# Performance work log

Measured on AMD Instinct MI355X. Metric: run time of the kernel, lower is better.

Reference implementation:

```python
import jax, jax.numpy as jnp
import numpy as np

H = 16        # num_attention_heads
KVH = 4       # num_key_value_heads
D = 128       # head_dim
K = 5         # query multiplier k
HID = 2048    # hidden_size = H * D
THETA = 10000.0


def rotate_half(x):
    h = x.shape[-1] // 2
    return jnp.concatenate([-x[..., h:], x[..., :h]], axis=-1)


def setup_inputs() -> dict:
    key = jax.random.key(0)
    ks = jax.random.split(key, 6)
    B, S = 1, 1024
    q_len = S - 1
    hidden_states = jax.random.normal(ks[0], (B, S, HID), jnp.float32)
    prev_hidden_states = jax.random.normal(ks[1], (B, S - 1, HID), jnp.float32)
    causal = jnp.tril(jnp.ones((q_len, q_len), bool))
    attention_mask = jnp.where(causal, 0.0, -1e9).astype(jnp.float32)[None, None]  # (1,1,q,kv)
    position_ids = jnp.arange(q_len, dtype=jnp.int64)[None]  # (1, kv_len)
    Wq = jax.random.normal(ks[2], (HID, H * D * K), jnp.float32) * 0.02
    Wkv = jax.random.normal(ks[3], (2 * HID, 2 * KVH * D), jnp.float32) * 0.02
    Wo = jax.random.normal(ks[4], (HID, HID), jnp.float32) * 0.02
    return {
        'hidden_states': hidden_states,
        'prev_hidden_states': prev_hidden_states,
        'attention_mask': attention_mask,
        'position_ids': position_ids,
        'Wq': Wq,
        'Wkv': Wkv,
        'Wo': Wo,
    }


def reference(hidden_states, prev_hidden_states, attention_mask, position_ids, Wq, Wkv, Wo):
    B = hidden_states.shape[0]  # must be 1 for this module's broadcasting
    # feature-dim concat of previous layer states with shifted current states
    prev = jnp.concatenate([prev_hidden_states, hidden_states[:, :-1]], axis=-1)  # (B, S-1, 2*HID)
    hs = hidden_states[:, 1:]  # training-mode slice -> (B, q_len, HID)
    q_len = hs.shape[1]
    kv_len = prev.shape[1]

    q = hs @ Wq                       # (B, q_len, H*D*K)
    kv = prev @ Wkv                   # (B, kv_len, 2*KVH*D)
    k_st, v_st = jnp.split(kv, 2, axis=-1)

    # faithful raw reshape: (B, q_len, H*D*K) -> (B*K, q_len, H, D) -> (B*K, H, q_len, D)
    q = q.reshape(B * K, -1, H, D).transpose(0, 2, 1, 3)
    k_st = k_st.reshape(B, kv_len, KVH, D).transpose(0, 2, 1, 3)   # (B, KVH, kv, D)
    v_st = v_st.reshape(B, kv_len, KVH, D).transpose(0, 2, 1, 3)

    # RoPE (LlamaRotaryEmbedding)
    inv_freq = 1.0 / (THETA ** (jnp.arange(0, D, 2, dtype=jnp.float32) / D))  # (D/2,)
    freqs = position_ids.astype(jnp.float32)[..., None] * inv_freq            # (B, kv, D/2)
    emb = jnp.concatenate([freqs, freqs], axis=-1)                            # (B, kv, D)
    cos = jnp.cos(emb)[:, None]  # (B, 1, kv, D)
    sin = jnp.sin(emb)[:, None]
    q = q * cos[..., -q_len:, :] + rotate_half(q) * sin[..., -q_len:, :]
    k_st = k_st * cos[..., :kv_len, :] + rotate_half(k_st) * sin[..., :kv_len, :]

    # repeat_kv: (B, KVH, kv, D) -> (B, H, kv, D)
    n_rep = H // KVH
    k_rep = jnp.repeat(k_st, n_rep, axis=1)
    v_rep = jnp.repeat(v_st, n_rep, axis=1)

    # (B*K, H, q, D) @ (B, H, D, kv) -> broadcast over k variants (B==1)
    attn = jnp.matmul(q, jnp.swapaxes(k_rep, -1, -2)) / jnp.sqrt(jnp.float32(D))
    attn = attn + attention_mask
    attn = jax.nn.softmax(attn.astype(jnp.float32), axis=-1).astype(q.dtype)
    out = jnp.matmul(attn, v_rep)                 # (B*K, H, q, D)
    out = out.transpose(0, 2, 1, 3).reshape(B * K, q_len, HID)
    return out @ Wo                                # (B*K, q_len, HID)
```

## Files before the change

kernel.cpp:

```cpp
#include <hip/hip_runtime.h>
#include <cstddef>
#include <cstdint>

#define SQ    1023
#define HIDC  2048
#define NQC   10240
#define NKVC  1024

typedef unsigned short ushort_t;
typedef __bf16 bf16x8 __attribute__((ext_vector_type(8)));
typedef float  f32x4  __attribute__((ext_vector_type(4)));

__device__ __forceinline__ ushort_t f2bf(float x) {
  union { float f; uint32_t u; } v; v.f = x;
  uint32_t r = v.u + 0x7fffu + ((v.u >> 16) & 1u);
  return (ushort_t)(r >> 16);
}

__device__ __forceinline__ ushort_t f2bf_fast(float x) {
  __bf16 b = (__bf16)x;
  return __builtin_bit_cast(ushort_t, b);
}

__device__ __forceinline__ float fexp2(float x) {
  float r;
  asm("v_exp_f32 %0, %1\n\ts_nop 0" : "=v"(r) : "v"(x));
  return r;
}

__device__ __forceinline__ void fexp2x4(float& a, float& b, float& c, float& d) {
  asm("v_exp_f32 %0, %0\n\t"
      "v_exp_f32 %1, %1\n\t"
      "v_exp_f32 %2, %2\n\t"
      "v_exp_f32 %3, %3\n\t"
      "s_nop 0"
      : "+v"(a), "+v"(b), "+v"(c), "+v"(d));
}

__device__ __forceinline__ void tconv_body(const float* __restrict__ in,
                                           ushort_t* __restrict__ out,
                                           int K, int N, int bx, int by,
                                           int tid, float (&t)[32][33]) {
  int n0 = bx * 32, k0 = by * 32;
  int r = tid >> 5, c = tid & 31;
  #pragma unroll
  for (int p = 0; p < 4; ++p)
    t[p * 8 + r][c] = in[(size_t)(k0 + p * 8 + r) * N + n0 + c];
  __syncthreads();
  #pragma unroll
  for (int p = 0; p < 4; ++p)
    out[(size_t)(n0 + p * 8 + r) * K + k0 + c] = f2bf(t[c][p * 8 + r]);
}

__global__ __launch_bounds__(256)
void k_pre(const float* __restrict__ Wq, const float* __restrict__ Wkv,
           const float* __restrict__ Wo, const float* __restrict__ hidden,
           const float* __restrict__ prevh,
           ushort_t* __restrict__ wqt, ushort_t* __restrict__ wkvt,
           ushort_t* __restrict__ wot, ushort_t* __restrict__ hbf,
           ushort_t* __restrict__ akv,
           float* __restrict__ cosT, float* __restrict__ sinT)
{
  __shared__ float tsh[32][33];
  const int tid = threadIdx.x;
  int b = blockIdx.x;
  if (b < 20480) { tconv_body(Wq, wqt, HIDC, NQC, b % 320, b / 320, tid, tsh); return; }
  b -= 20480;
  if (b < 4096)  { tconv_body(Wkv, wkvt, 4096, NKVC, b % 32, b / 32, tid, tsh); return; }
  b -= 4096;
  if (b < 4096)  { tconv_body(Wo, wot, HIDC, HIDC, b % 64, b / 64, tid, tsh); return; }
  b -= 4096;
  if (b < 2046) {
    int i = (b * 256 + tid) * 4;
    if (i >= SQ * 2048) return;
    int r = i >> 11, c = i & 2047;
    float4 h1 = *reinterpret_cast<const float4*>(hidden + (size_t)(r + 1) * 2048 + c);
    float4 h0 = *reinterpret_cast<const float4*>(hidden + (size_t)r * 2048 + c);
    float4 pv = *reinterpret_cast<const float4*>(prevh + (size_t)r * 2048 + c);
    uint2 a, bb, d;
    a.x  = (uint32_t)f2bf(h1.x) | ((uint32_t)f2bf(h1.y) << 16);
    a.y  = (uint32_t)f2bf(h1.z) | ((uint32_t)f2bf(h1.w) << 16);
    bb.x = (uint32_t)f2bf(pv.x) | ((uint32_t)f2bf(pv.y) << 16);
    bb.y = (uint32_t)f2bf(pv.z) | ((uint32_t)f2bf(pv.w) << 16);
    d.x  = (uint32_t)f2bf(h0.x) | ((uint32_t)f2bf(h0.y) << 16);
    d.y  = (uint32_t)f2bf(h0.z) | ((uint32_t)f2bf(h0.w) << 16);
    *reinterpret_cast<uint2*>(hbf + i) = a;
    *reinterpret_cast<uint2*>(akv + (size_t)r * 4096 + c) = bb;
    *reinterpret_cast<uint2*>(akv + (size_t)r * 4096 + 2048 + c) = d;
    return;
  }
  b -= 2046;
  {
    int idx = b * 256 + tid;
    if (idx >= SQ * 64) return;
    int t = idx >> 6, i = idx & 63;
    float inv = powf(10000.0f, -(float)i * (1.0f / 64.0f));
    float f = (float)t * inv;
    cosT[idx] = cosf(f);
    sinT[idx] = sinf(f);
  }
}

__global__ __launch_bounds__(256)
void k_gemms(const ushort_t* __restrict__ hbf, const ushort_t* __restrict__ wqt,
             ushort_t* __restrict__ qbb, const float* __restrict__ cosT,
             const float* __restrict__ sinT,
             const ushort_t* __restrict__ akv, const ushort_t* __restrict__ wkvt,
             float* __restrict__ kvp)
{
  __shared__ __align__(16) ushort_t As[3][128 * 32];
  __shared__ __align__(16) ushort_t Bs[3][128 * 32];

  const int tid  = threadIdx.x;
  const int lane = tid & 63;
  const int w    = tid >> 6;
  const int wm   = w >> 1, wn = w & 1;
  const int fr   = lane & 15;
  const int kg   = (lane >> 4) * 8;
  const int g4   = lane >> 4;
  const int lrow = lane >> 2;
  const int lk   = (lane & 3) * 8;

  if (blockIdx.x < 640) {
    const int Kd = 2048;
    const int m0 = (blockIdx.x / 80) * 128, n0 = (blockIdx.x % 80) * 128;
    const ushort_t* A  = hbf;
    const ushort_t* Bt = wqt;

    f32x4 acc[4][4];
    #pragma unroll
    for (int i = 0; i < 4; ++i)
      #pragma unroll
      for (int j = 0; j < 4; ++j) acc[i][j] = (f32x4){0.f, 0.f, 0.f, 0.f};

    auto STAGE = [&](int b, int k0) {
      #pragma unroll
      for (int c = 0; c < 2; ++c) {
        int ch  = w + c * 4;
        int row = ch * 16 + lrow;
        const ushort_t* ga = A  + (size_t)(m0 + row) * Kd + k0 + lk;
        const ushort_t* gb = Bt + (size_t)(n0 + row) * Kd + k0 + lk;
        __builtin_amdgcn_global_load_lds(
            (const __attribute__((address_space(1))) void*)ga,
            (__attribute__((address_space(3))) void*)(&As[b][0] + ch * 512), 16, 0, 0);
        __builtin_amdgcn_global_load_lds(
            (const __attribute__((address_space(1))) void*)gb,
            (__attribute__((address_space(3))) void*)(&Bs[b][0] + ch * 512), 16, 0, 0);
      }
    };

    const int nt = Kd / 32;
    STAGE(0, 0);
    STAGE(1, 32);

    int cur = 0;
    for (int t = 0; t < nt; ++t) {
      if (t + 1 < nt) {
        asm volatile("s_waitcnt vmcnt(4)" ::: "memory");
      } else {
        asm volatile("s_waitcnt vmcnt(0)" ::: "memory");
      }
      __builtin_amdgcn_s_barrier();
      if (t + 2 < nt) {
        int sb = cur + 2; if (sb >= 3) sb -= 3;
        STAGE(sb, (t + 2) * 32);
      }

      bf16x8 av[4], bv[4];
      #pragma unroll
      for (int mi = 0; mi < 4; ++mi)
        av[mi] = *reinterpret_cast<const bf16x8*>(&As[cur][0] + (wm * 64 + mi * 16 + fr) * 32 + kg);
      #pragma unroll
      for (int nj = 0; nj < 4; ++nj) {
        int colOff = wn * 32 + (nj & 1) * 16 + (nj >> 1) * 64;
        bv[nj] = *reinterpret_cast<const bf16x8*>(&Bs[cur][0] + (colOff + fr) * 32 + kg);
      }
      #pragma unroll
      for (int mi = 0; mi < 4; ++mi)
        #pragma unroll
        for (int nj = 0; nj < 4; ++nj)
          acc[mi][nj] = __builtin_amdgcn_mfma_f32_16x16x32_bf16(av[mi], bv[nj], acc[mi][nj], 0, 0, 0);

      cur = (cur == 2) ? 0 : cur + 1;
    }

    const float sc = 0.1275174485f;
    const int nChunk = n0 >> 11;
    #pragma unroll
    for (int mi = 0; mi < 4; ++mi) {
      #pragma unroll
      for (int r = 0; r < 4; ++r) {
        int gr = m0 + wm * 64 + mi * 16 + g4 * 4 + r;
        if (gr >= SQ) continue;
        int st  = gr * 5 + nChunk;
        int tau = st % 1023;
        const float* ct  = cosT + tau * 64;
        const float* stb = sinT + tau * 64;
        #pragma unroll
        for (int njp = 0; njp < 2; ++njp) {
          int dd = wn * 32 + njp * 16 + fr;
          float c = ct[dd], s = stb[dd];
          float x0 = acc[mi][njp][r];
          float x1 = acc[mi][njp + 2][r];
          size_t base = (size_t)gr * 10240 + n0 + dd;
          qbb[base]      = f2bf_fast((x0 * c - x1 * s) * sc);
          qbb[base + 64] = f2bf_fast((x1 * c + x0 * s) * sc);
        }
      }
    }
  } else {
    const int u = blockIdx.x - 640;
    const int Kd = 4096, M = SQ, N = NKVC, kLen = 1024;
    const int n0 = (u & 7) * 128, m0 = ((u >> 3) & 15) * 64;
    const int kOff = (u >> 7) * kLen;
    float* C = kvp + (size_t)(u >> 7) * M * N;
    ushort_t* As64 = &As[0][0];
    ushort_t* Bs64 = &Bs[0][0];

    const int arow = tid >> 2, aslot = (tid & 3) * 8;
    const int l15 = lane & 15;

    f32x4 acc[2][4];
    #pragma unroll
    for (int i = 0; i < 2; ++i)
      #pragma unroll
      for (int j = 0; j < 4; ++j) acc[i][j] = (f32x4){0.f, 0.f, 0.f, 0.f};

    for (int k0 = kOff; k0 < kOff + kLen; k0 += 32) {
      {
        const ushort_t* ga = akv + (size_t)(m0 + arow) * Kd + k0 + aslot;
        __builtin_amdgcn_global_load_lds(
            (const __attribute__((address_space(1))) void*)ga,
            (__attribute__((address_space(3))) void*)(As64 + w * 512), 16, 0, 0);
      }
      #pragma unroll
      for (int c = 0; c < 2; ++c) {
        int uu = c * 256 + tid;
        const ushort_t* gb = wkvt + (size_t)(n0 + (uu >> 2)) * Kd + k0 + (uu & 3) * 8;
        __builtin_amdgcn_global_load_lds(
            (const __attribute__((address_space(1))) void*)gb,
            (__attribute__((address_space(3))) void*)(Bs64 + (c * 256 + w * 64) * 8), 16, 0, 0);
      }
      __syncthreads();

      bf16x8 av[2], bv[4];
      #pragma unroll
      for (int mi = 0; mi < 2; ++mi)
        av[mi] = *reinterpret_cast<const bf16x8*>(As64 + (wm * 32 + mi * 16 + fr) * 32 + kg);
      #pragma unroll
      for (int nj = 0; nj < 4; ++nj)
        bv[nj] = *reinterpret_cast<const bf16x8*>(Bs64 + (wn * 64 + nj * 16 + fr) * 32 + kg);
      #pragma unroll
      for (int mi = 0; mi < 2; ++mi)
        #pragma unroll
        for (int nj = 0; nj < 4; ++nj)
          acc[mi][nj] = __builtin_amdgcn_mfma_f32_16x16x32_bf16(av[mi], bv[nj], acc[mi][nj], 0, 0, 0);
      __syncthreads();
    }

    #pragma unroll
    for (int mi = 0; mi < 2; ++mi) {
      #pragma unroll
      for (int nj = 0; nj < 4; ++nj) {
        int rbase = m0 + wm * 32 + mi * 16 + g4 * 4;
        int col   = n0 + wn * 64 + nj * 16 + l15;
        #pragma unroll
        for (int r = 0; r < 4; ++r) {
          int gr = rbase + r;
          if (gr < M) C[(size_t)gr * N + col] = acc[mi][nj][r];
        }
      }
    }
  }
}

__global__ __launch_bounds__(256)
void k_kv(const float* __restrict__ kvp, ushort_t* __restrict__ kb,
          ushort_t* __restrict__ vt, const float* __restrict__ cosT,
          const float* __restrict__ sinT)
{
  __shared__ float tile[32][33];
  const int tid = threadIdx.x;
  int b = blockIdx.x;
  if (b < 1023) {
    int idx = b * 256 + tid;
    if (idx >= SQ * 4 * 64) return;
    int d   = idx & 63;
    int kvh = (idx >> 6) & 3;
    int t   = idx >> 8;
    size_t src = (size_t)t * 1024 + kvh * 128 + d;
    float x0 = 0.f, x1 = 0.f;
    #pragma unroll
    for (int z = 0; z < 4; ++z) {
      x0 += kvp[(size_t)z * (SQ * 1024) + src];
      x1 += kvp[(size_t)z * (SQ * 1024) + src + 64];
    }
    float c = cosT[t * 64 + d], s = sinT[t * 64 + d];
    size_t dst = (size_t)t * 512 + kvh * 128 + d;
    kb[dst]      = f2bf(x0 * c - x1 * s);
    kb[dst + 64] = f2bf(x1 * c + x0 * s);
    return;
  }
  b -= 1023;
  {
    int v0 = (b & 15) * 32;
    int t0 = (b >> 4) * 32;
    int r = tid >> 5, c = tid & 31;
    #pragma unroll
    for (int p = 0; p < 4; ++p) {
      int t = t0 + p * 8 + r;
      float s = 0.f;
      if (t < SQ) {
        size_t src = (size_t)t * 1024 + 512 + v0 + c;
        #pragma unroll
        for (int z = 0; z < 4; ++z) s += kvp[(size_t)z * (SQ * 1024) + src];
      }
      tile[p * 8 + r][c] = s;
    }
    __syncthreads();
    #pragma unroll
    for (int p = 0; p < 4; ++p) {
      int v = v0 + p * 8 + r;
      vt[(size_t)v * 1024 + t0 + c] = f2bf(tile[c][p * 8 + r]);
    }
  }
}

__global__ __launch_bounds__(256)
void k_gemm3buf(const ushort_t* __restrict__ A, const ushort_t* __restrict__ Bt,
                float* __restrict__ C, int M, int N, int Kd)
{
  __shared__ __align__(16) ushort_t As[3][128 * 32];
  __shared__ __align__(16) ushort_t Bs[3][128 * 32];

  const int tid  = threadIdx.x;
  const int lane = tid & 63;
  const int w    = tid >> 6;
  const int wm   = w >> 1, wn = w & 1;
  const int fr   = lane & 15;
  const int kg   = (lane >> 4) * 8;
  const int m0   = blockIdx.y * 128, n0 = blockIdx.x * 128;

  const int lrow = lane >> 2;
  const int lk   = (lane & 3) * 8;

  f32x4 acc[4][4];
  #pragma unroll
  for (int i = 0; i < 4; ++i)
    #pragma unroll
    for (int j = 0; j < 4; ++j) acc[i][j] = (f32x4){0.f, 0.f, 0.f, 0.f};

  auto STAGE = [&](int b, int k0) {
    #pragma unroll
    for (int c = 0; c < 2; ++c) {
      int ch  = w + c * 4;
      int row = ch * 16 + lrow;
      const ushort_t* ga = A  + (size_t)(m0 + row) * Kd + k0 + lk;
      const ushort_t* gb = Bt + (size_t)(n0 + row) * Kd + k0 + lk;
      __builtin_amdgcn_global_load_lds(
          (const __attribute__((address_space(1))) void*)ga,
          (__attribute__((address_space(3))) void*)(&As[b][0] + ch * 512), 16, 0, 0);
      __builtin_amdgcn_global_load_lds(
          (const __attribute__((address_space(1))) void*)gb,
          (__attribute__((address_space(3))) void*)(&Bs[b][0] + ch * 512), 16, 0, 0);
    }
  };

  const int nt = Kd / 32;
  STAGE(0, 0);
  STAGE(1, 32);

  int cur = 0;
  for (int t = 0; t < nt; ++t) {
    if (t + 1 < nt) {
      asm volatile("s_waitcnt vmcnt(4)" ::: "memory");
    } else {
      asm volatile("s_waitcnt vmcnt(0)" ::: "memory");
    }
    __builtin_amdgcn_s_barrier();
    if (t + 2 < nt) {
      int sb = cur + 2; if (sb >= 3) sb -= 3;
      STAGE(sb, (t + 2) * 32);
    }

    bf16x8 av[4], bv[4];
    #pragma unroll
    for (int mi = 0; mi < 4; ++mi)
      av[mi] = *reinterpret_cast<const bf16x8*>(&As[cur][0] + (wm * 64 + mi * 16 + fr) * 32 + kg);
    #pragma unroll
    for (int nj = 0; nj < 4; ++nj)
      bv[nj] = *reinterpret_cast<const bf16x8*>(&Bs[cur][0] + (wn * 64 + nj * 16 + fr) * 32 + kg);
    #pragma unroll
    for (int mi = 0; mi < 4; ++mi)
      #pragma unroll
      for (int nj = 0; nj < 4; ++nj)
        acc[mi][nj] = __builtin_amdgcn_mfma_f32_16x16x32_bf16(av[mi], bv[nj], acc[mi][nj], 0, 0, 0);

    cur = (cur == 2) ? 0 : cur + 1;
  }

  #pragma unroll
  for (int mi = 0; mi < 4; ++mi) {
    #pragma unroll
    for (int nj = 0; nj < 4; ++nj) {
      int rbase = m0 + wm * 64 + mi * 16 + (lane >> 4) * 4;
      int col   = n0 + wn * 64 + nj * 16 + fr;
      #pragma unroll
      for (int r = 0; r < 4; ++r) {
        int gr = rbase + r;
        if (gr < M) C[(size_t)gr * N + col] = acc[mi][nj][r];
      }
    }
  }
}

__global__ __launch_bounds__(256)
void k_attn_mfma(const ushort_t* __restrict__ qb, const ushort_t* __restrict__ kb,
                 const ushort_t* __restrict__ vt, ushort_t* __restrict__ oattb)
{
  __shared__ __align__(16) ushort_t Ks[64 * 128];
  __shared__ __align__(16) ushort_t Vs[128 * 64];
  __shared__ __align__(16) ushort_t Ps[4][16 * 64];

  const int tid  = threadIdx.x;
  const int lane = tid & 63;
  const int w    = tid >> 6;
  const int l15  = lane & 15;
  const int g4   = lane >> 4;
  const int gh   = blockIdx.x;
  const int g = gh >> 4, h = gh & 15, kvh = (gh & 15) >> 2;
  const int qt = 15 - blockIdx.y;
  const int t0 = qt * 64;
  const int tq = t0 + w * 16 + l15;

  bf16x8 av[4];
  {
    const ushort_t* qrow = qb + (((size_t)(g * SQ + tq)) * 16 + h) * 128;
    #pragma unroll
    for (int kk = 0; kk < 4; ++kk)
      av[kk] = *reinterpret_cast<const bf16x8*>(qrow + kk * 32 + g4 * 8);
  }

  f32x4 acc[8];
  #pragma unroll
  for (int dt = 0; dt < 8; ++dt) acc[dt] = (f32x4){0.f, 0.f, 0.f, 0.f};
  float lsum = 0.f;
  float m = -1e30f;

  char* pwb = (char*)&Ps[w][0] + l15 * 128;
  const int pswz = (l15 & 7) << 4;

  for (int jt = 0; jt <= qt; ++jt) {
    int u0 = jt * 64;
    #pragma unroll
    for (int i = 0; i < 4; ++i) {
      int c = (w * 4 + i) * 64 + lane;
      int kv = c >> 4, sl = c & 15;
      const ushort_t* srck = kb + (size_t)(u0 + kv) * 512 + kvh * 128 + ((sl ^ (kv & 7)) << 3);
      __builtin_amdgcn_global_load_lds(
          (const __attribute__((address_space(1))) void*)srck,
          (__attribute__((address_space(3))) void*)(Ks + (w * 4 + i) * 512), 16, 0, 0);
      int d = c >> 3, sv = c & 7;
      const ushort_t* srcv = vt + (size_t)(kvh * 128 + d) * 1024 + u0 + ((sv ^ (d & 7)) << 3);
      __builtin_amdgcn_global_load_lds(
          (const __attribute__((address_space(1))) void*)srcv,
          (__attribute__((address_space(3))) void*)(Vs + (w * 4 + i) * 512), 16, 0, 0);
    }
    __syncthreads();

    f32x4 S[4];
    #pragma unroll
    for (int ct = 0; ct < 4; ++ct) S[ct] = (f32x4){0.f, 0.f, 0.f, 0.f};
    #pragma unroll
    for (int ct = 0; ct < 4; ++ct) {
      int kv = ct * 16 + l15;
      #pragma unroll
      for (int kk = 0; kk < 4; ++kk) {
        bf16x8 kvf = *reinterpret_cast<const bf16x8*>(
            Ks + kv * 128 + ((((kk << 2) | g4) ^ (kv & 7)) << 3));
        S[ct] = __builtin_amdgcn_mfma_f32_16x16x32_bf16(kvf, av[kk], S[ct], 0, 0, 0);
      }
    }
    if (jt == qt) {
      #pragma unroll
      for (int ct = 0; ct < 4; ++ct) {
        int ub = u0 + ct * 16 + g4 * 4;
        #pragma unroll
        for (int r = 0; r < 4; ++r)
          if (ub + r > tq) S[ct][r] = -1e30f;
      }
    }
    float a0 = fmaxf(fmaxf(S[0][0], S[0][1]), fmaxf(S[0][2], S[0][3]));
    float a1 = fmaxf(fmaxf(S[1][0], S[1][1]), fmaxf(S[1][2], S[1][3]));
    float a2 = fmaxf(fmaxf(S[2][0], S[2][1]), fmaxf(S[2][2], S[2][3]));
    float a3 = fmaxf(fmaxf(S[3][0], S[3][1]), fmaxf(S[3][2], S[3][3]));
    float tm = fmaxf(fmaxf(a0, a1), fmaxf(a2, a3));
    tm = fmaxf(tm, __shfl_xor(tm, 16));
    tm = fmaxf(tm, __shfl_xor(tm, 32));

    bool need = tm > m + 8.f;
    if (__any(need)) {
      float mn = fmaxf(m, tm);
      float corr = fexp2(m - mn);
      m = mn;
      lsum *= corr;
      #pragma unroll
      for (int dt = 0; dt < 8; ++dt) acc[dt] *= corr;
    }

    float ps = 0.f;
    #pragma unroll
    for (int ct = 0; ct < 4; ++ct) {
      float e0 = S[ct][0] - m;
      float e1 = S[ct][1] - m;
      float e2 = S[ct][2] - m;
      float e3 = S[ct][3] - m;
      fexp2x4(e0, e1, e2, e3);
      ps += (e0 + e1) + (e2 + e3);
      uint2 pv;
      pv.x = (uint32_t)f2bf_fast(e0) | ((uint32_t)f2bf_fast(e1) << 16);
      pv.y = (uint32_t)f2bf_fast(e2) | ((uint32_t)f2bf_fast(e3) << 16);
      *reinterpret_cast<uint2*>(pwb + ((ct * 32 + g4 * 8) ^ pswz)) = pv;
    }
    ps += __shfl_xor(ps, 16);
    ps += __shfl_xor(ps, 32);
    lsum += ps;

    #pragma unroll
    for (int kk = 0; kk < 2; ++kk) {
      bf16x8 pa = *reinterpret_cast<const bf16x8*>(pwb + ((kk * 64 + g4 * 16) ^ pswz));
      #pragma unroll
      for (int dt = 0; dt < 8; ++dt) {
        int d = dt * 16 + l15;
        bf16x8 vv = *reinterpret_cast<const bf16x8*>(
            Vs + d * 64 + ((((kk << 2) | g4) ^ (d & 7)) << 3));
        acc[dt] = __builtin_amdgcn_mfma_f32_16x16x32_bf16(vv, pa, acc[dt], 0, 0, 0);
      }
    }
    __syncthreads();
  }

  if (tq < SQ) {
    float inv = 1.f / lsum;
    ushort_t* dst = oattb + ((size_t)(g * SQ + tq)) * 2048 + h * 128;
    #pragma unroll
    for (int dt = 0; dt < 8; ++dt) {
      uint2 ov;
      ov.x = (uint32_t)f2bf_fast(acc[dt][0] * inv) | ((uint32_t)f2bf_fast(acc[dt][1] * inv) << 16);
      ov.y = (uint32_t)f2bf_fast(acc[dt][2] * inv) | ((uint32_t)f2bf_fast(acc[dt][3] * inv) << 16);
      *reinterpret_cast<uint2*>(dst + dt * 16 + g4 * 4) = ov;
    }
  }
}

extern "C" void kernel_launch(void* const* d_in, const int* in_sizes, int n_in,
                              void* d_out, int out_size, void* d_ws, size_t ws_size,
                              hipStream_t stream) {
  const float* hidden = (const float*)d_in[0];
  const float* prevh  = (const float*)d_in[1];
  const float* Wq     = (const float*)d_in[4];
  const float* Wkv    = (const float*)d_in[5];
  const float* Wo     = (const float*)d_in[6];
  float* out = (float*)d_out;

  char* ws = (char*)d_ws;
  float*    kvp   = (float*)ws;                        ws += (size_t)4 * SQ * 1024 * 4;
  float*    cosT  = (float*)ws;                        ws += (size_t)65472 * 4;
  float*    sinT  = (float*)ws;                        ws += (size_t)65472 * 4;
  ushort_t* qbb   = (ushort_t*)ws;                     ws += (size_t)5120 * 2048 * 2;
  ushort_t* kb    = (ushort_t*)ws;                     ws += (size_t)1024 * 512 * 2;
  ushort_t* vtb   = (ushort_t*)ws;                     ws += (size_t)512 * 1024 * 2;
  ushort_t* hbf   = (ushort_t*)ws;                     ws += (size_t)1024 * 2048 * 2;
  ushort_t* akv   = (ushort_t*)ws;                     ws += (size_t)1024 * 4096 * 2;
  ushort_t* oattb = (ushort_t*)ws;                     ws += (size_t)5120 * 2048 * 2;
  ushort_t* wqt   = (ushort_t*)ws;                     ws += (size_t)10240 * 2048 * 2;
  ushort_t* wkvt  = (ushort_t*)ws;                     ws += (size_t)1024 * 4096 * 2;
  ushort_t* wot   = (ushort_t*)ws;                     ws += (size_t)2048 * 2048 * 2;

  k_pre<<<dim3(20480 + 4096 + 4096 + 2046 + 256), dim3(256), 0, stream>>>(
      Wq, Wkv, Wo, hidden, prevh, wqt, wkvt, wot, hbf, akv, cosT, sinT);

  k_gemms<<<dim3(1152), dim3(256), 0, stream>>>(
      hbf, wqt, qbb, cosT, sinT, akv, wkvt, kvp);

  k_kv<<<dim3(1023 + 512), dim3(256), 0, stream>>>(kvp, kb, vtb, cosT, sinT);

  k_attn_mfma<<<dim3(80, 16), dim3(256), 0, stream>>>(qbb, kb, vtb, oattb);

  k_gemm3buf<<<dim3(HIDC / 128, 40), dim3(256), 0, stream>>>(oattb, wot, out, 5115, HIDC, 2048);
}
```

Baseline: 244.0 us.

## Split Q projection along K and move RoPE into attention Q load

The Q GEMM is split-K into two partial fp32 buffers when workspace allows, doubling its block count from 640 so the GPU has more parallelism. One partial is written into the output buffer as scratch. RoPE and the softmax scale move from the GEMM epilogue into the attention kernel, which sums the partials and rotates while loading Q. This adds fp32 write and read traffic of about 40MB per partial in exchange for better occupancy of the Q GEMM.

```diff
diff --git a/kernel.cpp b/kernel.cpp
--- a/kernel.cpp
+++ b/kernel.cpp
@@ -103,8 +103,7 @@
 
 __global__ __launch_bounds__(256)
 void k_gemms(const ushort_t* __restrict__ hbf, const ushort_t* __restrict__ wqt,
-             ushort_t* __restrict__ qbb, const float* __restrict__ cosT,
-             const float* __restrict__ sinT,
+             float* __restrict__ qp0, float* __restrict__ qp1, int zq,
              const ushort_t* __restrict__ akv, const ushort_t* __restrict__ wkvt,
              float* __restrict__ kvp)
 {
@@ -120,10 +119,16 @@
   const int g4   = lane >> 4;
   const int lrow = lane >> 2;
   const int lk   = (lane & 3) * 8;
-
-  if (blockIdx.x < 640) {
+  const int nG1  = 640 * zq;
+
+  if ((int)blockIdx.x < nG1) {
     const int Kd = 2048;
-    const int m0 = (blockIdx.x / 80) * 128, n0 = (blockIdx.x % 80) * 128;
+    const int z  = (int)blockIdx.x >= 640 ? 1 : 0;
+    const int b  = blockIdx.x - z * 640;
+    const int kLen = Kd / zq;
+    const int m0 = (b / 80) * 128, n0 = (b % 80) * 128;
+    const int kOff = z * kLen;
+    float* C = z ? qp1 : qp0;
     const ushort_t* A  = hbf;
     const ushort_t* Bt = wqt;
 
@@ -133,7 +138,7 @@
       #pragma unroll
       for (int j = 0; j < 4; ++j) acc[i][j] = (f32x4){0.f, 0.f, 0.f, 0.f};
 
-    auto STAGE = [&](int b, int k0) {
+    auto STAGE = [&](int bb, int k0) {
       #pragma unroll
       for (int c = 0; c < 2; ++c) {
         int ch  = w + c * 4;
@@ -142,16 +147,16 @@
         const ushort_t* gb = Bt + (size_t)(n0 + row) * Kd + k0 + lk;
         __builtin_amdgcn_global_load_lds(
             (const __attribute__((address_space(1))) void*)ga,
-            (__attribute__((address_space(3))) void*)(&As[b][0] + ch * 512), 16, 0, 0);
+            (__attribute__((address_space(3))) void*)(&As[bb][0] + ch * 512), 16, 0, 0);
         __builtin_amdgcn_global_load_lds(
             (const __attribute__((address_space(1))) void*)gb,
-            (__attribute__((address_space(3))) void*)(&Bs[b][0] + ch * 512), 16, 0, 0);
+            (__attribute__((address_space(3))) void*)(&Bs[bb][0] + ch * 512), 16, 0, 0);
       }
     };
 
-    const int nt = Kd / 32;
-    STAGE(0, 0);
-    STAGE(1, 32);
+    const int nt = kLen / 32;
+    STAGE(0, kOff);
+    STAGE(1, kOff + 32);
 
     int cur = 0;
     for (int t = 0; t < nt; ++t) {
@@ -163,7 +168,7 @@
       __builtin_amdgcn_s_barrier();
       if (t + 2 < nt) {
         int sb = cur + 2; if (sb >= 3) sb -= 3;
-        STAGE(sb, (t + 2) * 32);
+        STAGE(sb, kOff + (t + 2) * 32);
       }
 
       bf16x8 av[4], bv[4];
@@ -171,10 +176,8 @@
       for (int mi = 0; mi < 4; ++mi)
         av[mi] = *reinterpret_cast<const bf16x8*>(&As[cur][0] + (wm * 64 + mi * 16 + fr) * 32 + kg);
       #pragma unroll
-      for (int nj = 0; nj < 4; ++nj) {
-        int colOff = wn * 32 + (nj & 1) * 16 + (nj >> 1) * 64;
-        bv[nj] = *reinterpret_cast<const bf16x8*>(&Bs[cur][0] + (colOff + fr) * 32 + kg);
-      }
+      for (int nj = 0; nj < 4; ++nj)
+        bv[nj] = *reinterpret_cast<const bf16x8*>(&Bs[cur][0] + (wn * 64 + nj * 16 + fr) * 32 + kg);
       #pragma unroll
       for (int mi = 0; mi < 4; ++mi)
         #pragma unroll
@@ -184,32 +187,21 @@
       cur = (cur == 2) ? 0 : cur + 1;
     }
 
-    const float sc = 0.1275174485f;
-    const int nChunk = n0 >> 11;
     #pragma unroll
     for (int mi = 0; mi < 4; ++mi) {
       #pragma unroll
-      for (int r = 0; r < 4; ++r) {
-        int gr = m0 + wm * 64 + mi * 16 + g4 * 4 + r;
-        if (gr >= SQ) continue;
-        int st  = gr * 5 + nChunk;
-        int tau = st % 1023;
-        const float* ct  = cosT + tau * 64;
-        const float* stb = sinT + tau * 64;
+      for (int nj = 0; nj < 4; ++nj) {
+        int rbase = m0 + wm * 64 + mi * 16 + g4 * 4;
+        int col   = n0 + wn * 64 + nj * 16 + fr;
         #pragma unroll
-        for (int njp = 0; njp < 2; ++njp) {
-          int dd = wn * 32 + njp * 16 + fr;
-          float c = ct[dd], s = stb[dd];
-          float x0 = acc[mi][njp][r];
-          float x1 = acc[mi][njp + 2][r];
-          size_t base = (size_t)gr * 10240 + n0 + dd;
-          qbb[base]      = f2bf_fast((x0 * c - x1 * s) * sc);
-          qbb[base + 64] = f2bf_fast((x1 * c + x0 * s) * sc);
+        for (int r = 0; r < 4; ++r) {
+          int gr = rbase + r;
+          if (gr < SQ) C[(size_t)gr * 10240 + col] = acc[mi][nj][r];
         }
       }
     }
   } else {
-    const int u = blockIdx.x - 640;
+    const int u = blockIdx.x - nG1;
     const int Kd = 4096, M = SQ, N = NKVC, kLen = 1024;
     const int n0 = (u & 7) * 128, m0 = ((u >> 3) & 15) * 64;
     const int kOff = (u >> 7) * kLen;
@@ -415,8 +407,10 @@
 }
 
 __global__ __launch_bounds__(256)
-void k_attn_mfma(const ushort_t* __restrict__ qb, const ushort_t* __restrict__ kb,
-                 const ushort_t* __restrict__ vt, ushort_t* __restrict__ oattb)
+void k_attn_mfma(const float* __restrict__ qp0, const float* __restrict__ qp1,
+                 int zq, const ushort_t* __restrict__ kb,
+                 const ushort_t* __restrict__ vt, ushort_t* __restrict__ oattb,
+                 const float* __restrict__ cosT, const float* __restrict__ sinT)
 {
   __shared__ __align__(16) ushort_t Ks[64 * 128];
   __shared__ __align__(16) ushort_t Vs[128 * 64];
@@ -435,10 +429,33 @@
 
   bf16x8 av[4];
   {
-    const ushort_t* qrow = qb + (((size_t)(g * SQ + tq)) * 16 + h) * 128;
-    #pragma unroll
-    for (int kk = 0; kk < 4; ++kk)
-      av[kk] = *reinterpret_cast<const bf16x8*>(qrow + kk * 32 + g4 * 8);
+    const int tqc = (tq < SQ) ? tq : (SQ - 1);
+    const size_t qoff = ((size_t)(g * SQ + tqc)) * 2048 + h * 128 + g4 * 8;
+    float x[4][8];
+    #pragma unroll
+    for (int kk = 0; kk < 4; ++kk) {
+      f32x4 a0 = *reinterpret_cast<const f32x4*>(qp0 + qoff + kk * 32);
+      f32x4 a1 = *reinterpret_cast<const f32x4*>(qp0 + qoff + kk * 32 + 4);
+      if (zq > 1) {
+        a0 += *reinterpret_cast<const f32x4*>(qp1 + qoff + kk * 32);
+        a1 += *reinterpret_cast<const f32x4*>(qp1 + qoff + kk * 32 + 4);
+      }
+      #pragma unroll
+      for (int j = 0; j < 4; ++j) { x[kk][j] = a0[j]; x[kk][j + 4] = a1[j]; }
+    }
+    const float scq = 0.1275174485f;
+    const float* ct = cosT + tqc * 64 + g4 * 8;
+    const float* st = sinT + tqc * 64 + g4 * 8;
+    #pragma unroll
+    for (int kk = 0; kk < 2; ++kk) {
+      #pragma unroll
+      for (int j = 0; j < 8; ++j) {
+        float c = ct[kk * 32 + j], s = st[kk * 32 + j];
+        float x0 = x[kk][j], x1 = x[kk + 2][j];
+        av[kk][j]     = (__bf16)((x0 * c - x1 * s) * scq);
+        av[kk + 2][j] = (__bf16)((x1 * c + x0 * s) * scq);
+      }
+    }
   }
 
   f32x4 acc[8];
@@ -563,11 +580,11 @@
   const float* Wo     = (const float*)d_in[6];
   float* out = (float*)d_out;
 
-  char* ws = (char*)d_ws;
+  char* ws  = (char*)d_ws;
+  char* ws0 = ws;
   float*    kvp   = (float*)ws;                        ws += (size_t)4 * SQ * 1024 * 4;
   float*    cosT  = (float*)ws;                        ws += (size_t)65472 * 4;
   float*    sinT  = (float*)ws;                        ws += (size_t)65472 * 4;
-  ushort_t* qbb   = (ushort_t*)ws;                     ws += (size_t)5120 * 2048 * 2;
   ushort_t* kb    = (ushort_t*)ws;                     ws += (size_t)1024 * 512 * 2;
   ushort_t* vtb   = (ushort_t*)ws;                     ws += (size_t)512 * 1024 * 2;
   ushort_t* hbf   = (ushort_t*)ws;                     ws += (size_t)1024 * 2048 * 2;
@@ -576,16 +593,22 @@
   ushort_t* wqt   = (ushort_t*)ws;                     ws += (size_t)10240 * 2048 * 2;
   ushort_t* wkvt  = (ushort_t*)ws;                     ws += (size_t)1024 * 4096 * 2;
   ushort_t* wot   = (ushort_t*)ws;                     ws += (size_t)2048 * 2048 * 2;
+  float*    qp1   = (float*)ws;                        ws += (size_t)5120 * 2048 * 4;
+
+  const int zq = (ws_size >= (size_t)(ws - ws0)) ? 2 : 1;
+
+  float* qp0 = out;
 
   k_pre<<<dim3(20480 + 4096 + 4096 + 2046 + 256), dim3(256), 0, stream>>>(
       Wq, Wkv, Wo, hidden, prevh, wqt, wkvt, wot, hbf, akv, cosT, sinT);
 
-  k_gemms<<<dim3(1152), dim3(256), 0, stream>>>(
-      hbf, wqt, qbb, cosT, sinT, akv, wkvt, kvp);
+  k_gemms<<<dim3(640 * zq + 512), dim3(256), 0, stream>>>(
+      hbf, wqt, qp0, qp1, zq, akv, wkvt, kvp);
 
   k_kv<<<dim3(1023 + 512), dim3(256), 0, stream>>>(kvp, kb, vtb, cosT, sinT);
 
-  k_attn_mfma<<<dim3(80, 16), dim3(256), 0, stream>>>(qbb, kb, vtb, oattb);
+  k_attn_mfma<<<dim3(80, 16), dim3(256), 0, stream>>>(
+      qp0, qp1, zq, kb, vtb, oattb, cosT, sinT);
 
   k_gemm3buf<<<dim3(HIDC / 128, 40), dim3(256), 0, stream>>>(oattb, wot, out, 5115, HIDC, 2048);
 }
```

Result: slower. 255.8 us (+4.9%).
